# Kernel optimization log

Measured on AMD Instinct MI355X. Metric: run time of the kernel, lower is better.

The kernel has to match this reference:

```python
import jax, jax.numpy as jnp
import numpy as np


def _bce_logits(x, t):
    # numerically stable BCE-with-logits, elementwise
    return jnp.maximum(x, 0.0) - x * t + jnp.log1p(jnp.exp(-jnp.abs(x)))


def setup_inputs() -> dict:
    key = jax.random.key(0)
    k1, k2, k3, k4, k5 = jax.random.split(key, 5)
    B, A, H, W, C, N = 32, 3, 64, 64, 80, 2048
    pred = jax.random.normal(k1, (B, A, H, W, 5 + C), dtype=jnp.float32)
    tb = jax.random.randint(k2, (N, 1), 0, B).astype(jnp.float32)
    tl = jax.random.randint(k3, (N, 1), 0, C).astype(jnp.float32)
    txy = jax.random.uniform(k4, (N, 2), dtype=jnp.float32)
    twh = jax.random.uniform(k5, (N, 2), minval=0.02, maxval=0.98, dtype=jnp.float32)
    target = jnp.concatenate([tb, tl, txy, twh], axis=-1)  # [N,6]
    anchors = jnp.array([[10.0, 13.0], [33.0, 23.0], [62.0, 45.0]], dtype=jnp.float32)
    return {"pred": pred, "target": target, "anchors": anchors, "num_classes": C}


def reference(pred, target, anchors, num_classes):
    B, A, H, W, _ = pred.shape
    N = target.shape[0]
    # scale normalized xywh to grid units (grid size = pred.size(2) = H)
    t = jnp.concatenate([target[..., :2], target[..., 2:] * H], axis=-1)
    pred_bbox_all = pred[..., :4]
    pred_conf = pred[..., 4:5]          # [B,A,H,W,1]
    pred_cls_all = pred[..., 5:]
    b_idx = t[..., 0].astype(jnp.int32)
    labels = t[..., 1].astype(jnp.int32)
    target_xy = t[..., 2:4]
    target_wh = t[..., 4:6]
    w_idx = target_wh[..., 0].astype(jnp.int32)
    h_idx = target_wh[..., 1].astype(jnp.int32)
    # IoU of same-center (w,h) boxes: [A,N]
    inter = jnp.minimum(anchors[:, None, 0], target_wh[None, :, 0]) * \
            jnp.minimum(anchors[:, None, 1], target_wh[None, :, 1])
    area_a = (anchors[:, 0] * anchors[:, 1])[:, None]
    area_t = (target_wh[:, 0] * target_wh[:, 1])[None, :]
    ious = inter / (area_a + area_t - inter)
    iou_idx = jnp.argmax(ious, axis=0)  # [N]
    txy_frac = target_xy - jnp.floor(target_xy)
    twh_log = jnp.log(target_wh / anchors[iou_idx])
    target_bbox = jnp.concatenate([txy_frac, twh_log], axis=-1)  # [N,4]
    pred_bbox = pred_bbox_all[b_idx, iou_idx, h_idx, w_idx]      # [N,4]
    pred_cls = pred_cls_all[b_idx, iou_idx, h_idx, w_idx]        # [N,C]
    target_cls = jax.nn.one_hot(labels, num_classes, dtype=pred_cls.dtype)
    # obj / noobj masks over [B,A,H,W,1]
    obj = jnp.zeros((B, A, H, W), dtype=pred.dtype).at[b_idx, iou_idx, h_idx, w_idx].set(1.0)
    noobj = 1.0 - obj
    # zero noobj at (batch[i], a, h[i], w[i]) for every anchor a with iou > 0.5
    keep = (ious <= 0.5).astype(pred.dtype)                      # [A,N]
    a_grid = jnp.broadcast_to(jnp.arange(A)[:, None], (A, N))
    b_grid = jnp.broadcast_to(b_idx[None, :], (A, N))
    h_grid = jnp.broadcast_to(h_idx[None, :], (A, N))
    w_grid = jnp.broadcast_to(w_idx[None, :], (A, N))
    noobj = noobj.at[b_grid, a_grid, h_grid, w_grid].mul(keep)
    pc = pred_conf[..., 0]
    n_obj = jnp.sum(obj)
    n_noobj = jnp.sum(noobj)
    conf_sum = jnp.sum(obj * _bce_logits(pc, 1.0)) + jnp.sum(noobj * _bce_logits(pc, 0.0))
    loss_conf = conf_sum / (n_obj + n_noobj)
    loss_xywh = jnp.mean((pred_bbox - target_bbox) ** 2)
    loss_cls = jnp.mean(_bce_logits(pred_cls, target_cls))
    return loss_xywh + loss_conf + loss_cls
```

## Files before the change

kernel.cpp:

```cpp
#include <hip/hip_runtime.h>
#include <math.h>

#define BB 32
#define AA 3
#define HH 64
#define WW 64
#define CC 80
#define NN 2048
#define CH (5 + CC)
#define NCELL (BB * AA * HH * WW)

#define CELL_BLOCKS (NCELL / 256)
#define TGT_BLOCKS  (NN / 4)
#define TOTAL_BLOCKS (CELL_BLOCKS + TGT_BLOCKS)

#define OBJ_BIT 1u
#define SUP_BIT 4u

__device__ __forceinline__ float bce_pos(float x) {
    return fmaxf(x, 0.f) - x + log1pf(expf(-fabsf(x)));
}
__device__ __forceinline__ float bce_neg(float x) {
    return fmaxf(x, 0.f) + log1pf(expf(-fabsf(x)));
}

__device__ __forceinline__ float wave_reduce(float v) {
    #pragma unroll
    for (int off = 32; off > 0; off >>= 1) v += __shfl_down(v, off, 64);
    return v;
}


__global__ void yolo_mega(const float* __restrict__ pred,
                          const float* __restrict__ target,
                          const float* __restrict__ anchors,
                          unsigned int* __restrict__ mask,
                          float* __restrict__ partial) {
    __shared__ float s_red[4][5];
    int wave = threadIdx.x >> 6, lane = threadIdx.x & 63;
    float cs = 0.f, dob = 0.f, dno = 0.f, lx = 0.f, lc = 0.f;

    if (blockIdx.x < CELL_BLOCKS) {
        int cell = blockIdx.x * 256 + threadIdx.x;
        float x = pred[(long)cell * CH + 4];
        cs = bce_neg(x);
    } else {
        int n = (blockIdx.x - CELL_BLOCKS) * 4 + wave;

        float tx = target[n * 6 + 2] * (float)HH;
        float ty = target[n * 6 + 3] * (float)HH;
        float tw = target[n * 6 + 4] * (float)HH;
        float th = target[n * 6 + 5] * (float)HH;
        int b     = (int)target[n * 6 + 0];
        int label = (int)target[n * 6 + 1];
        int wi = (int)tw;
        int hi = (int)th;

        float area_t = tw * th;
        float ious[AA];
        float best = -1.f;
        int bi = 0;
        #pragma unroll
        for (int a = 0; a < AA; a++) {
            float aw = anchors[a * 2 + 0];
            float ah = anchors[a * 2 + 1];
            float inter = fminf(aw, tw) * fminf(ah, th);
            float iou = inter / (aw * ah + area_t - inter);
            ious[a] = iou;
            if (iou > best) { best = iou; bi = a; }
        }

        if (lane < AA) {
            int a = lane;
            unsigned int bits = 0u;
            if (a == bi) bits |= OBJ_BIT;
            if (ious[a] > 0.5f) bits |= SUP_BIT;
            if (bits) {
                int cell = ((b * AA + a) * HH + hi) * WW + wi;
                unsigned int old = atomicOr(&mask[cell], bits) & (OBJ_BIT | SUP_BIT);
                unsigned int nw = old | bits;
                if (nw != old) {
                    float x = pred[(long)cell * CH + 4];
                    float neg = bce_neg(x), pos = bce_pos(x);
                    float fo_c = (old & OBJ_BIT) ? pos : ((old & SUP_BIT) ? 0.f : neg);
                    float fn_c = (nw  & OBJ_BIT) ? pos : ((nw  & SUP_BIT) ? 0.f : neg);
                    cs  = fn_c - fo_c;
                    dob = ((nw & OBJ_BIT) ? 1.f : 0.f) - ((old & OBJ_BIT) ? 1.f : 0.f);
                    dno = -((old == 0u) ? 1.f : 0.f);
                }
            }
        }

        long pbase = (long)(((b * AA + bi) * HH + hi) * WW + wi) * CH;

        if (lane < 4) {
            float t0 = tx - floorf(tx);
            float t1 = ty - floorf(ty);
            float t2 = logf(tw / anchors[bi * 2 + 0]);
            float t3 = logf(th / anchors[bi * 2 + 1]);
            float tt = (lane == 0) ? t0 : (lane == 1) ? t1 : (lane == 2) ? t2 : t3;
            float d = pred[pbase + lane] - tt;
            lx = d * d;
        }
        {
            float x = pred[pbase + 5 + lane];
            lc = (lane == label) ? bce_pos(x) : bce_neg(x);
            if (lane < CC - 64) {
                int c2 = 64 + lane;
                float x2 = pred[pbase + 5 + c2];
                lc += (c2 == label) ? bce_pos(x2) : bce_neg(x2);
            }
        }
    }

    cs  = wave_reduce(cs);
    dob = wave_reduce(dob);
    dno = wave_reduce(dno);
    lx  = wave_reduce(lx);
    lc  = wave_reduce(lc);
    if (lane == 0) {
        s_red[wave][0] = cs; s_red[wave][1] = dob; s_red[wave][2] = dno;
        s_red[wave][3] = lx; s_red[wave][4] = lc;
    }
    __syncthreads();
    if (threadIdx.x < 5) {
        int j = threadIdx.x;
        partial[blockIdx.x * 5 + j] =
            s_red[0][j] + s_red[1][j] + s_red[2][j] + s_red[3][j];
    }
}

__global__ void yolo_finalize(const float* __restrict__ partial,
                              float* __restrict__ out) {
    __shared__ float s_red[4][5];
    int wave = threadIdx.x >> 6, lane = threadIdx.x & 63;
    float v[5] = {0.f, 0.f, 0.f, 0.f, 0.f};
    for (int i = threadIdx.x; i < TOTAL_BLOCKS; i += 256) {
        #pragma unroll
        for (int j = 0; j < 5; j++) v[j] += partial[i * 5 + j];
    }
    #pragma unroll
    for (int j = 0; j < 5; j++) v[j] = wave_reduce(v[j]);
    if (lane == 0) {
        #pragma unroll
        for (int j = 0; j < 5; j++) s_red[wave][j] = v[j];
    }
    __syncthreads();
    if (threadIdx.x == 0) {
        float cs  = s_red[0][0] + s_red[1][0] + s_red[2][0] + s_red[3][0];
        float dob = s_red[0][1] + s_red[1][1] + s_red[2][1] + s_red[3][1];
        float dno = s_red[0][2] + s_red[1][2] + s_red[2][2] + s_red[3][2];
        float lx  = s_red[0][3] + s_red[1][3] + s_red[2][3] + s_red[3][3];
        float lc  = s_red[0][4] + s_red[1][4] + s_red[2][4] + s_red[3][4];
        float n_obj   = dob;
        float n_noobj = (float)NCELL + dno;
        float loss_xywh = lx / ((float)NN * 4.f);
        float loss_cls  = lc / ((float)NN * (float)CC);
        float loss_conf = cs / (n_obj + n_noobj);
        out[0] = loss_xywh + loss_conf + loss_cls;
    }
}

extern "C" void kernel_launch(void* const* d_in, const int* in_sizes, int n_in,
                              void* d_out, int out_size, void* d_ws, size_t ws_size,
                              hipStream_t stream) {
    const float* pred    = (const float*)d_in[0];
    const float* target  = (const float*)d_in[1];
    const float* anchors = (const float*)d_in[2];
    (void)in_sizes; (void)n_in; (void)out_size; (void)ws_size;

    unsigned int* mask = (unsigned int*)d_ws;
    float* partial     = (float*)((char*)d_ws + (size_t)NCELL * 4);


    yolo_mega<<<TOTAL_BLOCKS, 256, 0, stream>>>(pred, target, anchors, mask, partial);
    yolo_finalize<<<1, 256, 0, stream>>>(partial, (float*)d_out);
}
```

Before: 186.4 us.

## Stream whole pred tensor with coalesced float4 loads to extract confidence channel

Replaces the one-thread-per-cell strided read of the confidence channel with a grid-stride pass over the entire pred tensor using float4 loads. Each thread uses a modulo-85 test to pick out the confidence element, if any, inside each vector. The aim is to turn scattered 340-byte-stride accesses into fully coalesced streaming reads. The cost is that about 20x more bytes are read from memory, plus an integer modulo per vector.

```diff
diff --git a/kernel.cpp b/kernel.cpp
--- a/kernel.cpp
+++ b/kernel.cpp
@@ -9,10 +9,14 @@
 #define NN 2048
 #define CH (5 + CC)
 #define NCELL (BB * AA * HH * WW)
+#define NFLOAT (NCELL * CH)
+#define NF4 (NFLOAT / 4)
 
-#define CELL_BLOCKS (NCELL / 256)
+#define STREAM_BLOCKS 2048
+#define STREAM_THREADS (STREAM_BLOCKS * 256)
+#define STREAM_ITERS ((NF4 + STREAM_THREADS - 1) / STREAM_THREADS)
 #define TGT_BLOCKS  (NN / 4)
-#define TOTAL_BLOCKS (CELL_BLOCKS + TGT_BLOCKS)
+#define TOTAL_BLOCKS (STREAM_BLOCKS + TGT_BLOCKS)
 
 #define OBJ_BIT 1u
 #define SUP_BIT 4u
@@ -40,12 +44,24 @@
     int wave = threadIdx.x >> 6, lane = threadIdx.x & 63;
     float cs = 0.f, dob = 0.f, dno = 0.f, lx = 0.f, lc = 0.f;
 
-    if (blockIdx.x < CELL_BLOCKS) {
-        int cell = blockIdx.x * 256 + threadIdx.x;
-        float x = pred[(long)cell * CH + 4];
-        cs = bce_neg(x);
+    if (blockIdx.x < STREAM_BLOCKS) {
+        const float4* p4 = reinterpret_cast<const float4*>(pred);
+        int gid = blockIdx.x * 256 + threadIdx.x;
+        #pragma unroll
+        for (int k = 0; k < STREAM_ITERS; k++) {
+            int idx = k * STREAM_THREADS + gid;
+            if (idx < NF4) {
+                float4 v = p4[idx];
+                unsigned int r = ((unsigned)idx * 4u) % 85u;
+                if (r >= 1u && r <= 4u) {
+                    float sel = (r == 1u) ? v.w : (r == 2u) ? v.z
+                              : (r == 3u) ? v.y : v.x;
+                    cs += bce_neg(sel);
+                }
+            }
+        }
     } else {
-        int n = (blockIdx.x - CELL_BLOCKS) * 4 + wave;
+        int n = (blockIdx.x - STREAM_BLOCKS) * 4 + wave;
 
         float tx = target[n * 6 + 2] * (float)HH;
         float ty = target[n * 6 + 3] * (float)HH;
```

Measured after the change: 199.9 us. 1.07x slower.
